# Kernel optimization log

Hardware: AMD Instinct MI355X
Metric: run time of the kernel (lower is better)

The kernel has to match this reference:

```python
import jax, jax.numpy as jnp
import numpy as np

N, D_MODEL, D_FFN, K = 8192, 1024, 4096, 512


def setup_inputs() -> dict:
    key = jax.random.key(0)
    ks = jax.random.split(key, 5)
    x = jax.random.normal(ks[0], (N, D_MODEL), dtype=jnp.float32)
    topk_indices = jax.random.randint(ks[1], (N, K), 0, D_FFN, dtype=jnp.int32)
    scale = 0.02
    w_gate = jax.random.normal(ks[2], (D_MODEL, D_FFN), dtype=jnp.float32) * scale
    w_up = jax.random.normal(ks[3], (D_MODEL, D_FFN), dtype=jnp.float32) * scale
    w_down = jax.random.normal(ks[4], (D_FFN, D_MODEL), dtype=jnp.float32) * scale
    return {"x": x, "topk_indices": topk_indices, "w_gate": w_gate, "w_up": w_up, "w_down": w_down}


def reference(x, topk_indices, w_gate, w_up, w_down):
    # Dense gate/up projections: [N, d_ffn]
    G = x @ w_gate
    U = x @ w_up
    # Gather only the top-k active neurons per token and fuse SwiGLU there.
    G_act = jnp.take_along_axis(G, topk_indices, axis=1)  # [N, k]
    U_act = jnp.take_along_axis(U, topk_indices, axis=1)  # [N, k]
    Z_active = jax.nn.silu(G_act) * U_act                 # [N, k]
    # Sparse-to-dense down projection: scatter active activations back into
    # the d_ffn axis (zeros elsewhere), then dense matmul with w_down.
    n, k = topk_indices.shape
    rows = jnp.arange(n, dtype=topk_indices.dtype)[:, None]
    Z_dense = jnp.zeros((n, w_down.shape[0]), dtype=Z_active.dtype).at[rows, topk_indices].add(Z_active)
    return Z_dense @ w_down  # [N, d_model]
```

## Files before the change

### kernel.cpp

```cpp
#include <hip/hip_runtime.h>
#include <hip/hip_bf16.h>
#include <cstdint>
#include <cstddef>

#define N_TOK   8192
#define D_MODEL 1024
#define D_FFN   4096
#define K_TOP   512
#define NHALF   2048

typedef __bf16 bf16_t;
typedef __bf16 bf16x8 __attribute__((ext_vector_type(8)));
typedef __bf16 bf16x4 __attribute__((ext_vector_type(4)));
typedef float  f32x4  __attribute__((ext_vector_type(4)));


__global__ void cvt_f32_bf16(const float* __restrict__ in, bf16_t* __restrict__ out, int n4) {
  int i = blockIdx.x * blockDim.x + threadIdx.x;
  if (i < n4) {
    const f32x4 v = ((const f32x4*)in)[i];
    bf16x4 o;
    o[0] = (bf16_t)v[0]; o[1] = (bf16_t)v[1]; o[2] = (bf16_t)v[2]; o[3] = (bf16_t)v[3];
    ((bf16x4*)out)[i] = o;
  }
}

__global__ void transpose_cvt(const float* __restrict__ in, bf16_t* __restrict__ out,
                              int rows, int cols) {
  __shared__ float tile[32][33];
  const int tx = threadIdx.x, ty = threadIdx.y;
  const int x = blockIdx.x * 32 + tx;
#pragma unroll
  for (int i = 0; i < 32; i += 8) {
    int y = blockIdx.y * 32 + ty + i;
    tile[ty + i][tx] = in[(size_t)y * cols + x];
  }
  __syncthreads();
  const int xo = blockIdx.y * 32 + tx;
#pragma unroll
  for (int i = 0; i < 32; i += 8) {
    int yo = blockIdx.x * 32 + ty + i;
    out[(size_t)yo * rows + xo] = (bf16_t)tile[tx][ty + i];
  }
}

#define ROWS_PER_BLK 4
__global__ __launch_bounds__(256) void count_scatter_lds(
    const int* __restrict__ idx, unsigned int* __restrict__ M) {
  __shared__ unsigned int loc[ROWS_PER_BLK * (D_FFN / 8)];
  const int t = threadIdx.x;
  const int r0 = blockIdx.x * ROWS_PER_BLK;

#pragma unroll
  for (int i = 0; i < ROWS_PER_BLK * (D_FFN / 8) / 256; ++i)
    loc[t + i * 256] = 0;
  __syncthreads();

  const int* ip = idx + (size_t)r0 * K_TOP;
#pragma unroll
  for (int i = 0; i < ROWS_PER_BLK * K_TOP / 256; ++i) {
    const int e = t + i * 256;
    const int lr = e >> 9;
    const int j = ip[e];
    atomicAdd(&loc[lr * (D_FFN / 8) + (j >> 3)], 1u << ((j & 7) * 4));
  }
  __syncthreads();

  unsigned int* op = M + (size_t)r0 * (D_FFN / 8);
#pragma unroll
  for (int i = 0; i < ROWS_PER_BLK * (D_FFN / 8) / 256; ++i)
    op[t + i * 256] = loc[t + i * 256];
}


__device__ __forceinline__ void gload_lds16(const void* g, void* l) {
#if __has_builtin(__builtin_amdgcn_global_load_lds)
  __builtin_amdgcn_global_load_lds((__attribute__((address_space(1))) void*)(g),
                                   (__attribute__((address_space(3))) void*)(l), 16, 0, 0);
#else
  *(bf16x8*)l = *(const bf16x8*)g;
#endif
}

#define MFMA16(ACC, AF, BF)                                                      \
  _Pragma("unroll")                                                              \
  for (int m = 0; m < 4; ++m)                                                    \
    _Pragma("unroll")                                                            \
    for (int n = 0; n < 4; ++n)                                                  \
      ACC[m][n] = __builtin_amdgcn_mfma_f32_16x16x32_bf16(AF[m], BF[n], ACC[m][n], 0, 0, 0);


#define BM1 256
#define BN1 128
#define BK1 32
#define NT1 (D_MODEL / BK1)
#define GU_BUF 32768

__global__ __launch_bounds__(512, 2) void gemm_gateup_3b(
    const bf16_t* __restrict__ A,
    const bf16_t* __restrict__ Bg,
    const bf16_t* __restrict__ Bu,
    const unsigned int* __restrict__ cnt,
    bf16_t* __restrict__ Z,
    int n_base)
{
  extern __shared__ char smem[];
  const int t = threadIdx.x;
  const int lane = t & 63;
  const int w = t >> 6;
  const int wr = w >> 1;
  const int wc = w & 1;
  const int l15 = lane & 15;
  const int grp = lane >> 4;
  const int m0 = blockIdx.x * BM1;
  const int n0 = blockIdx.y * BN1;

  const int sA0 = t, sA1 = t + 512;
  const int rA0 = sA0 >> 2, uA0 = (sA0 & 3) ^ ((rA0 >> 1) & 3);
  const int rA1 = sA1 >> 2, uA1 = (sA1 & 3) ^ ((rA1 >> 1) & 3);
  const int rB  = t >> 2,   uB  = (t & 3) ^ ((rB >> 1) & 3);
  const int gA0 = (m0 + rA0) * D_MODEL + uA0 * 8;
  const int gA1 = (m0 + rA1) * D_MODEL + uA1 * 8;
  const int gB  = (n_base + n0 + rB) * D_MODEL + uB * 8;
  const int dA0 = sA0 * 16, dA1 = sA1 * 16, dB = t * 16;

#define GU_STAGE(ti) do {                                                        \
    char* _b = smem + ((ti) % 3) * GU_BUF; const int _k = (ti) * BK1;            \
    gload_lds16(A  + gA0 + _k, _b + dA0);                                        \
    gload_lds16(A  + gA1 + _k, _b + dA1);                                        \
    gload_lds16(Bg + gB  + _k, _b + 16384 + dB);                                 \
    gload_lds16(Bu + gB  + _k, _b + 24576 + dB); } while (0)

  int a_off[4], bg_off[4];
#pragma unroll
  for (int m = 0; m < 4; ++m) {
    const int row = wr * 64 + m * 16 + l15;
    a_off[m] = row * 64 + ((grp ^ ((row >> 1) & 3)) * 16);
  }
#pragma unroll
  for (int n = 0; n < 4; ++n) {
    const int row = wc * 64 + n * 16 + l15;
    bg_off[n] = 16384 + row * 64 + ((grp ^ ((row >> 1) & 3)) * 16);
  }

  GU_STAGE(0); GU_STAGE(1);
  asm volatile("s_waitcnt vmcnt(4)" ::: "memory");
  __builtin_amdgcn_s_barrier();

  bf16x8 af[4], bgf[4], buf_[4];
#pragma unroll
  for (int m = 0; m < 4; ++m) af[m] = *(const bf16x8*)(smem + a_off[m]);
#pragma unroll
  for (int n = 0; n < 4; ++n) bgf[n] = *(const bf16x8*)(smem + bg_off[n]);

  f32x4 accg[4][4] = {};
  f32x4 accu[4][4] = {};

  for (int tt = 0; tt < NT1; ++tt) {
    char* rbuf = smem + (tt % 3) * GU_BUF;
    if (tt + 2 < NT1) GU_STAGE(tt + 2);
#pragma unroll
    for (int n = 0; n < 4; ++n) buf_[n] = *(const bf16x8*)(rbuf + bg_off[n] + 8192);
    asm volatile("s_waitcnt lgkmcnt(4)" ::: "memory");
    __builtin_amdgcn_s_setprio(1);
    MFMA16(accg, af, bgf);
    __builtin_amdgcn_s_setprio(0);
    asm volatile("s_waitcnt lgkmcnt(0)" ::: "memory");
    if (tt + 2 < NT1) { asm volatile("s_waitcnt vmcnt(4)" ::: "memory"); }
    else              { asm volatile("s_waitcnt vmcnt(0)" ::: "memory"); }
    __builtin_amdgcn_s_barrier();
    char* nbuf = smem + ((tt + 1) % 3) * GU_BUF;
    if (tt + 1 < NT1) {
#pragma unroll
      for (int n = 0; n < 4; ++n) bgf[n] = *(const bf16x8*)(nbuf + bg_off[n]);
    }
    __builtin_amdgcn_s_setprio(1);
    MFMA16(accu, af, buf_);
    __builtin_amdgcn_s_setprio(0);
    if (tt + 1 < NT1) {
#pragma unroll
      for (int m = 0; m < 4; ++m) af[m] = *(const bf16x8*)(nbuf + a_off[m]);
    }
  }

#pragma unroll
  for (int m = 0; m < 4; ++m) {
#pragma unroll
    for (int n = 0; n < 4; ++n) {
      const int colL = n0 + wc * 64 + n * 16 + l15;
      const int jg = n_base + colL;
#pragma unroll
      for (int j = 0; j < 4; ++j) {
        const int row = m0 + wr * 64 + m * 16 + grp * 4 + j;
        float g = accg[m][n][j];
        float u = accu[m][n][j];
        unsigned int cw = cnt[(size_t)row * (D_FFN / 8) + (jg >> 3)];
        float c = (float)((cw >> ((jg & 7) * 4)) & 15u);
        float z = c * u * (g / (1.0f + __expf(-g)));
        Z[(size_t)row * NHALF + colL] = (bf16_t)z;
      }
    }
  }
#undef GU_STAGE
}

#define BM2 256
#define BN2 128
#define BK2 32
#define NT2 (NHALF / BK2)
#define DN_BUF 24576

__global__ __launch_bounds__(512, 4) void gemm_down_3b(
    const bf16_t* __restrict__ Az,
    const bf16_t* __restrict__ B,
    float* __restrict__ C,
    int k_base, int accum)
{
  extern __shared__ char smem[];
  const int t = threadIdx.x;
  const int lane = t & 63;
  const int w = t >> 6;
  const int wr = w >> 1;
  const int wc = w & 1;
  const int l15 = lane & 15;
  const int grp = lane >> 4;
  const int m0 = blockIdx.x * BM2;
  const int n0 = blockIdx.y * BN2;

  const int sA0 = t, sA1 = t + 512;
  const int rA0 = sA0 >> 2, uA0 = (sA0 & 3) ^ ((rA0 >> 1) & 3);
  const int rA1 = sA1 >> 2, uA1 = (sA1 & 3) ^ ((rA1 >> 1) & 3);
  const int rB  = t >> 2,   uB  = (t & 3) ^ ((rB >> 1) & 3);
  const int gA0 = (m0 + rA0) * NHALF + uA0 * 8;
  const int gA1 = (m0 + rA1) * NHALF + uA1 * 8;
  const int gB  = (n0 + rB) * D_FFN + k_base + uB * 8;
  const int dA0 = sA0 * 16, dA1 = sA1 * 16, dB = t * 16;

#define DN_STAGE(ti) do {                                                        \
    char* _b = smem + ((ti) % 3) * DN_BUF; const int _k = (ti) * BK2;            \
    gload_lds16(Az + gA0 + _k, _b + dA0);                                        \
    gload_lds16(Az + gA1 + _k, _b + dA1);                                        \
    gload_lds16(B  + gB  + _k, _b + 16384 + dB); } while (0)

  int a_off[4], b_off[4];
#pragma unroll
  for (int m = 0; m < 4; ++m) {
    const int row = wr * 64 + m * 16 + l15;
    a_off[m] = row * 64 + ((grp ^ ((row >> 1) & 3)) * 16);
  }
#pragma unroll
  for (int n = 0; n < 4; ++n) {
    const int row = wc * 64 + n * 16 + l15;
    b_off[n] = 16384 + row * 64 + ((grp ^ ((row >> 1) & 3)) * 16);
  }

  DN_STAGE(0); DN_STAGE(1);
  asm volatile("s_waitcnt vmcnt(3)" ::: "memory");
  __builtin_amdgcn_s_barrier();

  bf16x8 af[4], bf[4];
#pragma unroll
  for (int m = 0; m < 4; ++m) af[m] = *(const bf16x8*)(smem + a_off[m]);
#pragma unroll
  for (int n = 0; n < 4; ++n) bf[n] = *(const bf16x8*)(smem + b_off[n]);

  f32x4 acc[4][4] = {};

  for (int tt = 0; tt < NT2; ++tt) {
    if (tt + 2 < NT2) DN_STAGE(tt + 2);
    __builtin_amdgcn_s_setprio(1);
    MFMA16(acc, af, bf);
    __builtin_amdgcn_s_setprio(0);
    asm volatile("s_waitcnt lgkmcnt(0)" ::: "memory");
    if (tt + 2 < NT2) { asm volatile("s_waitcnt vmcnt(3)" ::: "memory"); }
    else              { asm volatile("s_waitcnt vmcnt(0)" ::: "memory"); }
    __builtin_amdgcn_s_barrier();
    if (tt + 1 < NT2) {
      char* nbuf = smem + ((tt + 1) % 3) * DN_BUF;
#pragma unroll
      for (int m = 0; m < 4; ++m) af[m] = *(const bf16x8*)(nbuf + a_off[m]);
#pragma unroll
      for (int n = 0; n < 4; ++n) bf[n] = *(const bf16x8*)(nbuf + b_off[n]);
    }
  }

#pragma unroll
  for (int m = 0; m < 4; ++m) {
#pragma unroll
    for (int n = 0; n < 4; ++n) {
      const int col = n0 + wc * 64 + n * 16 + l15;
#pragma unroll
      for (int j = 0; j < 4; ++j) {
        const int row = m0 + wr * 64 + m * 16 + grp * 4 + j;
        const size_t off = (size_t)row * D_MODEL + col;
        float prev = accum ? C[off] : 0.0f;
        C[off] = prev + acc[m][n][j];
      }
    }
  }
#undef DN_STAGE
}


extern "C" void kernel_launch(void* const* d_in, const int* in_sizes, int n_in,
                              void* d_out, int out_size, void* d_ws, size_t ws_size,
                              hipStream_t stream) {
  const float* x  = (const float*)d_in[0];
  const int*   idx = (const int*)d_in[1];
  const float* wg = (const float*)d_in[2];
  const float* wu = (const float*)d_in[3];
  const float* wd = (const float*)d_in[4];
  float* out = (float*)d_out;

  char* ws = (char*)d_ws;
  const size_t SZ_XB  = (size_t)N_TOK * D_MODEL * 2;
  const size_t SZ_W   = (size_t)D_MODEL * D_FFN * 2;
  const size_t SZ_CNT = (size_t)N_TOK * D_FFN / 2;
  bf16_t* xb  = (bf16_t*)(ws);
  bf16_t* wgT = (bf16_t*)(ws + SZ_XB);
  bf16_t* wuT = (bf16_t*)(ws + SZ_XB + SZ_W);
  bf16_t* wdT = (bf16_t*)(ws + SZ_XB + 2 * SZ_W);
  unsigned int* cnt = (unsigned int*)(ws + SZ_XB + 3 * SZ_W);
  bf16_t* Z   = (bf16_t*)(ws + SZ_XB + 3 * SZ_W + SZ_CNT);

  (void)hipFuncSetAttribute((const void*)gemm_gateup_3b,
                            hipFuncAttributeMaxDynamicSharedMemorySize, 3 * GU_BUF);
  (void)hipFuncSetAttribute((const void*)gemm_down_3b,
                            hipFuncAttributeMaxDynamicSharedMemorySize, 3 * DN_BUF);

  count_scatter_lds<<<N_TOK / ROWS_PER_BLK, 256, 0, stream>>>(idx, cnt);
  cvt_f32_bf16<<<(N_TOK * D_MODEL / 4 + 255) / 256, 256, 0, stream>>>(x, xb, N_TOK * D_MODEL / 4);
  transpose_cvt<<<dim3(D_FFN / 32, D_MODEL / 32), dim3(32, 8), 0, stream>>>(wg, wgT, D_MODEL, D_FFN);
  transpose_cvt<<<dim3(D_FFN / 32, D_MODEL / 32), dim3(32, 8), 0, stream>>>(wu, wuT, D_MODEL, D_FFN);
  transpose_cvt<<<dim3(D_MODEL / 32, D_FFN / 32), dim3(32, 8), 0, stream>>>(wd, wdT, D_FFN, D_MODEL);

  gemm_gateup_3b<<<dim3(N_TOK / BM1, NHALF / BN1), 512, 3 * GU_BUF, stream>>>(xb, wgT, wuT, cnt, Z, 0);
  gemm_down_3b<<<dim3(N_TOK / BM2, D_MODEL / BN2), 512, 3 * DN_BUF, stream>>>(Z, wdT, out, 0, 0);
  gemm_gateup_3b<<<dim3(N_TOK / BM1, NHALF / BN1), 512, 3 * GU_BUF, stream>>>(xb, wgT, wuT, cnt, Z, NHALF);
  gemm_down_3b<<<dim3(N_TOK / BM2, D_MODEL / BN2), 512, 3 * DN_BUF, stream>>>(Z, wdT, out, NHALF, 1);
}
```

Measured before the change: 270.0 us.

## Load A fragments directly from global into registers, stage only B in LDS

Both GEMM kernels stop staging the activation (A) tile through LDS. Each wave now loads its A fragments straight from global memory one iteration ahead, while only the weight tiles go through the triple-buffered LDS ring. The aim is to shrink the LDS footprint and LDS traffic and to move the barrier to the loop head. The cost is that each A element is fetched by both waves sharing a row, and loads are less coalesced with global latency exposed. The down kernel's launch bound is also lowered from 4 to 2 blocks.

```diff
diff --git a/kernel.cpp b/kernel.cpp
--- a/kernel.cpp
+++ b/kernel.cpp
@@ -94,9 +94,9 @@
 #define BN1 128
 #define BK1 32
 #define NT1 (D_MODEL / BK1)
-#define GU_BUF 32768
-
-__global__ __launch_bounds__(512, 2) void gemm_gateup_3b(
+#define GU_BUF 16384
+
+__global__ __launch_bounds__(512, 2) void gemm_gateup_ad(
     const bf16_t* __restrict__ A,
     const bf16_t* __restrict__ Bg,
     const bf16_t* __restrict__ Bu,
@@ -115,41 +115,33 @@
   const int m0 = blockIdx.x * BM1;
   const int n0 = blockIdx.y * BN1;
 
-  const int sA0 = t, sA1 = t + 512;
-  const int rA0 = sA0 >> 2, uA0 = (sA0 & 3) ^ ((rA0 >> 1) & 3);
-  const int rA1 = sA1 >> 2, uA1 = (sA1 & 3) ^ ((rA1 >> 1) & 3);
-  const int rB  = t >> 2,   uB  = (t & 3) ^ ((rB >> 1) & 3);
-  const int gA0 = (m0 + rA0) * D_MODEL + uA0 * 8;
-  const int gA1 = (m0 + rA1) * D_MODEL + uA1 * 8;
-  const int gB  = (n_base + n0 + rB) * D_MODEL + uB * 8;
-  const int dA0 = sA0 * 16, dA1 = sA1 * 16, dB = t * 16;
+  const int rB = t >> 2, uB = (t & 3) ^ ((rB >> 1) & 3);
+  const int gB = (n_base + n0 + rB) * D_MODEL + uB * 8;
+  const int dB = t * 16;
 
 #define GU_STAGE(ti) do {                                                        \
     char* _b = smem + ((ti) % 3) * GU_BUF; const int _k = (ti) * BK1;            \
-    gload_lds16(A  + gA0 + _k, _b + dA0);                                        \
-    gload_lds16(A  + gA1 + _k, _b + dA1);                                        \
-    gload_lds16(Bg + gB  + _k, _b + 16384 + dB);                                 \
-    gload_lds16(Bu + gB  + _k, _b + 24576 + dB); } while (0)
-
-  int a_off[4], bg_off[4];
-#pragma unroll
-  for (int m = 0; m < 4; ++m) {
-    const int row = wr * 64 + m * 16 + l15;
-    a_off[m] = row * 64 + ((grp ^ ((row >> 1) & 3)) * 16);
-  }
+    gload_lds16(Bg + gB + _k, _b + dB);                                          \
+    gload_lds16(Bu + gB + _k, _b + 8192 + dB); } while (0)
+
+  const bf16_t* aP[4];
+#pragma unroll
+  for (int m = 0; m < 4; ++m)
+    aP[m] = A + (size_t)(m0 + wr * 64 + m * 16 + l15) * D_MODEL + grp * 8;
+
+  int bg_off[4];
 #pragma unroll
   for (int n = 0; n < 4; ++n) {
     const int row = wc * 64 + n * 16 + l15;
-    bg_off[n] = 16384 + row * 64 + ((grp ^ ((row >> 1) & 3)) * 16);
+    bg_off[n] = row * 64 + ((grp ^ ((row >> 1) & 3)) * 16);
   }
 
   GU_STAGE(0); GU_STAGE(1);
-  asm volatile("s_waitcnt vmcnt(4)" ::: "memory");
+  bf16x8 af[4], bgf[4];
+#pragma unroll
+  for (int m = 0; m < 4; ++m) af[m] = *(const bf16x8*)(aP[m]);
+  asm volatile("s_waitcnt vmcnt(6)" ::: "memory");
   __builtin_amdgcn_s_barrier();
-
-  bf16x8 af[4], bgf[4], buf_[4];
-#pragma unroll
-  for (int m = 0; m < 4; ++m) af[m] = *(const bf16x8*)(smem + a_off[m]);
 #pragma unroll
   for (int n = 0; n < 4; ++n) bgf[n] = *(const bf16x8*)(smem + bg_off[n]);
 
@@ -158,28 +150,39 @@
 
   for (int tt = 0; tt < NT1; ++tt) {
     char* rbuf = smem + (tt % 3) * GU_BUF;
-    if (tt + 2 < NT1) GU_STAGE(tt + 2);
-#pragma unroll
-    for (int n = 0; n < 4; ++n) buf_[n] = *(const bf16x8*)(rbuf + bg_off[n] + 8192);
+    const bool stg = (tt + 2 < NT1);
+    const bool nxt = (tt + 1 < NT1);
+
+    asm volatile("s_waitcnt vmcnt(4)" ::: "memory");
+    __builtin_amdgcn_s_barrier();
+    if (stg) GU_STAGE(tt + 2);
+    bf16x8 bu_[4];
+#pragma unroll
+    for (int n = 0; n < 4; ++n) bu_[n] = *(const bf16x8*)(rbuf + bg_off[n] + 8192);
     asm volatile("s_waitcnt lgkmcnt(4)" ::: "memory");
     __builtin_amdgcn_s_setprio(1);
     MFMA16(accg, af, bgf);
     __builtin_amdgcn_s_setprio(0);
-    asm volatile("s_waitcnt lgkmcnt(0)" ::: "memory");
-    if (tt + 2 < NT1) { asm volatile("s_waitcnt vmcnt(4)" ::: "memory"); }
-    else              { asm volatile("s_waitcnt vmcnt(0)" ::: "memory"); }
-    __builtin_amdgcn_s_barrier();
-    char* nbuf = smem + ((tt + 1) % 3) * GU_BUF;
-    if (tt + 1 < NT1) {
-#pragma unroll
-      for (int n = 0; n < 4; ++n) bgf[n] = *(const bf16x8*)(nbuf + bg_off[n]);
+
+    bf16x8 afN[4], bgfN[4];
+    if (nxt) {
+      char* nbuf = smem + ((tt + 1) % 3) * GU_BUF;
+#pragma unroll
+      for (int n = 0; n < 4; ++n) bgfN[n] = *(const bf16x8*)(nbuf + bg_off[n]);
+#pragma unroll
+      for (int m = 0; m < 4; ++m) afN[m] = *(const bf16x8*)(aP[m] + (tt + 1) * BK1);
+      asm volatile("s_waitcnt lgkmcnt(4)" ::: "memory");
+    } else {
+      asm volatile("s_waitcnt lgkmcnt(0)" ::: "memory");
     }
     __builtin_amdgcn_s_setprio(1);
-    MFMA16(accu, af, buf_);
+    MFMA16(accu, af, bu_);
     __builtin_amdgcn_s_setprio(0);
-    if (tt + 1 < NT1) {
-#pragma unroll
-      for (int m = 0; m < 4; ++m) af[m] = *(const bf16x8*)(nbuf + a_off[m]);
+    if (nxt) {
+#pragma unroll
+      for (int m = 0; m < 4; ++m) af[m] = afN[m];
+#pragma unroll
+      for (int n = 0; n < 4; ++n) bgf[n] = bgfN[n];
     }
   }
 
@@ -208,9 +211,9 @@
 #define BN2 128
 #define BK2 32
 #define NT2 (NHALF / BK2)
-#define DN_BUF 24576
-
-__global__ __launch_bounds__(512, 4) void gemm_down_3b(
+#define DN_BUF 8192
+
+__global__ __launch_bounds__(512, 2) void gemm_down_ad(
     const bf16_t* __restrict__ Az,
     const bf16_t* __restrict__ B,
     float* __restrict__ C,
@@ -227,60 +230,61 @@
   const int m0 = blockIdx.x * BM2;
   const int n0 = blockIdx.y * BN2;
 
-  const int sA0 = t, sA1 = t + 512;
-  const int rA0 = sA0 >> 2, uA0 = (sA0 & 3) ^ ((rA0 >> 1) & 3);
-  const int rA1 = sA1 >> 2, uA1 = (sA1 & 3) ^ ((rA1 >> 1) & 3);
-  const int rB  = t >> 2,   uB  = (t & 3) ^ ((rB >> 1) & 3);
-  const int gA0 = (m0 + rA0) * NHALF + uA0 * 8;
-  const int gA1 = (m0 + rA1) * NHALF + uA1 * 8;
-  const int gB  = (n0 + rB) * D_FFN + k_base + uB * 8;
-  const int dA0 = sA0 * 16, dA1 = sA1 * 16, dB = t * 16;
+  const int rB = t >> 2, uB = (t & 3) ^ ((rB >> 1) & 3);
+  const int gB = (n0 + rB) * D_FFN + k_base + uB * 8;
+  const int dB = t * 16;
 
 #define DN_STAGE(ti) do {                                                        \
-    char* _b = smem + ((ti) % 3) * DN_BUF; const int _k = (ti) * BK2;            \
-    gload_lds16(Az + gA0 + _k, _b + dA0);                                        \
-    gload_lds16(Az + gA1 + _k, _b + dA1);                                        \
-    gload_lds16(B  + gB  + _k, _b + 16384 + dB); } while (0)
-
-  int a_off[4], b_off[4];
-#pragma unroll
-  for (int m = 0; m < 4; ++m) {
-    const int row = wr * 64 + m * 16 + l15;
-    a_off[m] = row * 64 + ((grp ^ ((row >> 1) & 3)) * 16);
-  }
+    gload_lds16(B + gB + (ti) * BK2, smem + ((ti) % 3) * DN_BUF + dB); } while (0)
+
+  const bf16_t* aP[4];
+#pragma unroll
+  for (int m = 0; m < 4; ++m)
+    aP[m] = Az + (size_t)(m0 + wr * 64 + m * 16 + l15) * NHALF + grp * 8;
+
+  int b_off[4];
 #pragma unroll
   for (int n = 0; n < 4; ++n) {
     const int row = wc * 64 + n * 16 + l15;
-    b_off[n] = 16384 + row * 64 + ((grp ^ ((row >> 1) & 3)) * 16);
+    b_off[n] = row * 64 + ((grp ^ ((row >> 1) & 3)) * 16);
   }
 
   DN_STAGE(0); DN_STAGE(1);
-  asm volatile("s_waitcnt vmcnt(3)" ::: "memory");
+  bf16x8 af[4], bf[4];
+#pragma unroll
+  for (int m = 0; m < 4; ++m) af[m] = *(const bf16x8*)(aP[m]);
+  asm volatile("s_waitcnt vmcnt(5)" ::: "memory");
   __builtin_amdgcn_s_barrier();
-
-  bf16x8 af[4], bf[4];
-#pragma unroll
-  for (int m = 0; m < 4; ++m) af[m] = *(const bf16x8*)(smem + a_off[m]);
 #pragma unroll
   for (int n = 0; n < 4; ++n) bf[n] = *(const bf16x8*)(smem + b_off[n]);
 
   f32x4 acc[4][4] = {};
 
   for (int tt = 0; tt < NT2; ++tt) {
-    if (tt + 2 < NT2) DN_STAGE(tt + 2);
+    const bool stg = (tt + 2 < NT2);
+    const bool nxt = (tt + 1 < NT2);
+
+    asm volatile("s_waitcnt vmcnt(4)" ::: "memory");
+    __builtin_amdgcn_s_barrier();
+    if (stg) DN_STAGE(tt + 2);
+    asm volatile("s_waitcnt lgkmcnt(0)" ::: "memory");
+
+    bf16x8 afN[4], bfN[4];
+    if (nxt) {
+      char* nbuf = smem + ((tt + 1) % 3) * DN_BUF;
+#pragma unroll
+      for (int n = 0; n < 4; ++n) bfN[n] = *(const bf16x8*)(nbuf + b_off[n]);
+#pragma unroll
+      for (int m = 0; m < 4; ++m) afN[m] = *(const bf16x8*)(aP[m] + (tt + 1) * BK2);
+    }
     __builtin_amdgcn_s_setprio(1);
     MFMA16(acc, af, bf);
     __builtin_amdgcn_s_setprio(0);
-    asm volatile("s_waitcnt lgkmcnt(0)" ::: "memory");
-    if (tt + 2 < NT2) { asm volatile("s_waitcnt vmcnt(3)" ::: "memory"); }
-    else              { asm volatile("s_waitcnt vmcnt(0)" ::: "memory"); }
-    __builtin_amdgcn_s_barrier();
-    if (tt + 1 < NT2) {
-      char* nbuf = smem + ((tt + 1) % 3) * DN_BUF;
-#pragma unroll
-      for (int m = 0; m < 4; ++m) af[m] = *(const bf16x8*)(nbuf + a_off[m]);
-#pragma unroll
-      for (int n = 0; n < 4; ++n) bf[n] = *(const bf16x8*)(nbuf + b_off[n]);
+    if (nxt) {
+#pragma unroll
+      for (int m = 0; m < 4; ++m) af[m] = afN[m];
+#pragma unroll
+      for (int n = 0; n < 4; ++n) bf[n] = bfN[n];
     }
   }
 
@@ -323,9 +327,9 @@
   unsigned int* cnt = (unsigned int*)(ws + SZ_XB + 3 * SZ_W);
   bf16_t* Z   = (bf16_t*)(ws + SZ_XB + 3 * SZ_W + SZ_CNT);
 
-  (void)hipFuncSetAttribute((const void*)gemm_gateup_3b,
+  (void)hipFuncSetAttribute((const void*)gemm_gateup_ad,
                             hipFuncAttributeMaxDynamicSharedMemorySize, 3 * GU_BUF);
-  (void)hipFuncSetAttribute((const void*)gemm_down_3b,
+  (void)hipFuncSetAttribute((const void*)gemm_down_ad,
                             hipFuncAttributeMaxDynamicSharedMemorySize, 3 * DN_BUF);
 
   count_scatter_lds<<<N_TOK / ROWS_PER_BLK, 256, 0, stream>>>(idx, cnt);
@@ -334,8 +338,8 @@
   transpose_cvt<<<dim3(D_FFN / 32, D_MODEL / 32), dim3(32, 8), 0, stream>>>(wu, wuT, D_MODEL, D_FFN);
   transpose_cvt<<<dim3(D_MODEL / 32, D_FFN / 32), dim3(32, 8), 0, stream>>>(wd, wdT, D_FFN, D_MODEL);
 
-  gemm_gateup_3b<<<dim3(N_TOK / BM1, NHALF / BN1), 512, 3 * GU_BUF, stream>>>(xb, wgT, wuT, cnt, Z, 0);
-  gemm_down_3b<<<dim3(N_TOK / BM2, D_MODEL / BN2), 512, 3 * DN_BUF, stream>>>(Z, wdT, out, 0, 0);
-  gemm_gateup_3b<<<dim3(N_TOK / BM1, NHALF / BN1), 512, 3 * GU_BUF, stream>>>(xb, wgT, wuT, cnt, Z, NHALF);
-  gemm_down_3b<<<dim3(N_TOK / BM2, D_MODEL / BN2), 512, 3 * DN_BUF, stream>>>(Z, wdT, out, NHALF, 1);
-}
+  gemm_gateup_ad<<<dim3(N_TOK / BM1, NHALF / BN1), 512, 3 * GU_BUF, stream>>>(xb, wgT, wuT, cnt, Z, 0);
+  gemm_down_ad<<<dim3(N_TOK / BM2, D_MODEL / BN2), 512, 3 * DN_BUF, stream>>>(Z, wdT, out, 0, 0);
+  gemm_gateup_ad<<<dim3(N_TOK / BM1, NHALF / BN1), 512, 3 * GU_BUF, stream>>>(xb, wgT, wuT, cnt, Z, NHALF);
+  gemm_down_ad<<<dim3(N_TOK / BM2, D_MODEL / BN2), 512, 3 * DN_BUF, stream>>>(Z, wdT, out, NHALF, 1);
+}
```

Result: slower. 447.8 us (+65.9%).

## Restructure down-projection GEMM to double-buffered BK=64 pipeline with split-K sub-steps

Applied to the files above, without the earlier changes.

Replaces the triple-buffered BK=32 down-projection kernel with a double-buffered BK=64 variant. Each iteration prefetches the next tile and runs two MFMA sub-steps from the current LDS buffer, with barriers and sched_barrier fences controlling interleaving. It uses an 8-way XOR swizzle for the wider rows. The goal is fewer loop iterations and barrier/wait overheads per unit of MFMA work, at the cost of more LDS per block (96KB) and lower occupancy (launch bounds 2 instead of 4). It also adds extra barriers that could serialize waves.

```diff
diff --git a/kernel.cpp b/kernel.cpp
--- a/kernel.cpp
+++ b/kernel.cpp
@@ -206,12 +206,12 @@
 
 #define BM2 256
 #define BN2 128
-#define BK2 32
+#define BK2 64
 #define NT2 (NHALF / BK2)
-#define DN_BUF 24576
-
-__global__ __launch_bounds__(512, 4) void gemm_down_3b(
-    const bf16_t* __restrict__ Az,
+#define LDSBUF2 49152
+
+__global__ __launch_bounds__(512, 2) void gemm_down_8p(
+    const bf16_t* __restrict__ A,
     const bf16_t* __restrict__ B,
     float* __restrict__ C,
     int k_base, int accum)
@@ -227,61 +227,75 @@
   const int m0 = blockIdx.x * BM2;
   const int n0 = blockIdx.y * BN2;
 
-  const int sA0 = t, sA1 = t + 512;
-  const int rA0 = sA0 >> 2, uA0 = (sA0 & 3) ^ ((rA0 >> 1) & 3);
-  const int rA1 = sA1 >> 2, uA1 = (sA1 & 3) ^ ((rA1 >> 1) & 3);
-  const int rB  = t >> 2,   uB  = (t & 3) ^ ((rB >> 1) & 3);
-  const int gA0 = (m0 + rA0) * NHALF + uA0 * 8;
-  const int gA1 = (m0 + rA1) * NHALF + uA1 * 8;
-  const int gB  = (n0 + rB) * D_FFN + k_base + uB * 8;
-  const int dA0 = sA0 * 16, dA1 = sA1 * 16, dB = t * 16;
-
-#define DN_STAGE(ti) do {                                                        \
-    char* _b = smem + ((ti) % 3) * DN_BUF; const int _k = (ti) * BK2;            \
-    gload_lds16(Az + gA0 + _k, _b + dA0);                                        \
-    gload_lds16(Az + gA1 + _k, _b + dA1);                                        \
-    gload_lds16(B  + gB  + _k, _b + 16384 + dB); } while (0)
-
-  int a_off[4], b_off[4];
-#pragma unroll
-  for (int m = 0; m < 4; ++m) {
-    const int row = wr * 64 + m * 16 + l15;
-    a_off[m] = row * 64 + ((grp ^ ((row >> 1) & 3)) * 16);
-  }
-#pragma unroll
-  for (int n = 0; n < 4; ++n) {
-    const int row = wc * 64 + n * 16 + l15;
-    b_off[n] = 16384 + row * 64 + ((grp ^ ((row >> 1) & 3)) * 16);
-  }
-
-  DN_STAGE(0); DN_STAGE(1);
-  asm volatile("s_waitcnt vmcnt(3)" ::: "memory");
-  __builtin_amdgcn_s_barrier();
-
-  bf16x8 af[4], bf[4];
-#pragma unroll
-  for (int m = 0; m < 4; ++m) af[m] = *(const bf16x8*)(smem + a_off[m]);
-#pragma unroll
-  for (int n = 0; n < 4; ++n) bf[n] = *(const bf16x8*)(smem + b_off[n]);
+  int offA[4], offB[2];
+#pragma unroll
+  for (int c = 0; c < 4; ++c) {
+    const int s = c * 512 + w * 64 + lane;
+    const int r = s >> 3, cb = (s & 7) ^ (r & 7);
+    offA[c] = (m0 + r) * NHALF + cb * 8;
+  }
+#pragma unroll
+  for (int c = 0; c < 2; ++c) {
+    const int s = c * 512 + w * 64 + lane;
+    const int r = s >> 3, cb = (s & 7) ^ (r & 7);
+    offB[c] = (n0 + r) * D_FFN + k_base + cb * 8;
+  }
+  const int dst0 = (w * 64 + lane) * 16;
+
+  const int swz = l15 & 7;
+  const int a_k0 = wr * 8192 + l15 * 128 + ((0 + grp) ^ swz) * 16;
+  const int a_k1 = wr * 8192 + l15 * 128 + ((4 + grp) ^ swz) * 16;
+  const int b_k0 = 32768 + wc * 8192 + l15 * 128 + ((0 + grp) ^ swz) * 16;
+  const int b_k1 = 32768 + wc * 8192 + l15 * 128 + ((4 + grp) ^ swz) * 16;
+
+#pragma unroll
+  for (int c = 0; c < 4; ++c) gload_lds16(A + offA[c], smem + dst0 + c * 8192);
+#pragma unroll
+  for (int c = 0; c < 2; ++c) gload_lds16(B + offB[c], smem + 32768 + dst0 + c * 8192);
 
   f32x4 acc[4][4] = {};
 
   for (int tt = 0; tt < NT2; ++tt) {
-    if (tt + 2 < NT2) DN_STAGE(tt + 2);
+    char* rb = smem + (tt & 1) * LDSBUF2;
+    char* wb = smem + ((tt & 1) ^ 1) * LDSBUF2;
+    const int kg = (tt + 1) * BK2;
+    const bool st = (tt + 1 < NT2);
+    bf16x8 af[4], bf[4];
+
+    if (st) {
+#pragma unroll
+      for (int c = 0; c < 4; ++c) gload_lds16(A + offA[c] + kg, wb + dst0 + c * 8192);
+#pragma unroll
+      for (int c = 0; c < 2; ++c) gload_lds16(B + offB[c] + kg, wb + 32768 + dst0 + c * 8192);
+      asm volatile("s_waitcnt vmcnt(6)" ::: "memory");
+    } else {
+      asm volatile("s_waitcnt vmcnt(0)" ::: "memory");
+    }
+    __builtin_amdgcn_s_barrier();
+
+#pragma unroll
+    for (int m = 0; m < 4; ++m) af[m] = *(const bf16x8*)(rb + a_k0 + m * 2048);
+#pragma unroll
+    for (int n = 0; n < 4; ++n) bf[n] = *(const bf16x8*)(rb + b_k0 + n * 2048);
+    __builtin_amdgcn_s_barrier();
+    asm volatile("s_waitcnt lgkmcnt(0)" ::: "memory");
+    __builtin_amdgcn_sched_barrier(0);
     __builtin_amdgcn_s_setprio(1);
     MFMA16(acc, af, bf);
     __builtin_amdgcn_s_setprio(0);
+    __builtin_amdgcn_s_barrier();
+
+#pragma unroll
+    for (int m = 0; m < 4; ++m) af[m] = *(const bf16x8*)(rb + a_k1 + m * 2048);
+#pragma unroll
+    for (int n = 0; n < 4; ++n) bf[n] = *(const bf16x8*)(rb + b_k1 + n * 2048);
+    __builtin_amdgcn_s_barrier();
     asm volatile("s_waitcnt lgkmcnt(0)" ::: "memory");
-    if (tt + 2 < NT2) { asm volatile("s_waitcnt vmcnt(3)" ::: "memory"); }
-    else              { asm volatile("s_waitcnt vmcnt(0)" ::: "memory"); }
-    __builtin_amdgcn_s_barrier();
-    if (tt + 1 < NT2) {
-      char* nbuf = smem + ((tt + 1) % 3) * DN_BUF;
-#pragma unroll
-      for (int m = 0; m < 4; ++m) af[m] = *(const bf16x8*)(nbuf + a_off[m]);
-#pragma unroll
-      for (int n = 0; n < 4; ++n) bf[n] = *(const bf16x8*)(nbuf + b_off[n]);
-    }
+    __builtin_amdgcn_sched_barrier(0);
+    __builtin_amdgcn_s_setprio(1);
+    MFMA16(acc, af, bf);
+    __builtin_amdgcn_s_setprio(0);
+    __builtin_amdgcn_s_barrier();
   }
 
 #pragma unroll
@@ -298,7 +312,6 @@
       }
     }
   }
-#undef DN_STAGE
 }
 
 
@@ -325,8 +338,8 @@
 
   (void)hipFuncSetAttribute((const void*)gemm_gateup_3b,
                             hipFuncAttributeMaxDynamicSharedMemorySize, 3 * GU_BUF);
-  (void)hipFuncSetAttribute((const void*)gemm_down_3b,
-                            hipFuncAttributeMaxDynamicSharedMemorySize, 3 * DN_BUF);
+  (void)hipFuncSetAttribute((const void*)gemm_down_8p,
+                            hipFuncAttributeMaxDynamicSharedMemorySize, 2 * LDSBUF2);
 
   count_scatter_lds<<<N_TOK / ROWS_PER_BLK, 256, 0, stream>>>(idx, cnt);
   cvt_f32_bf16<<<(N_TOK * D_MODEL / 4 + 255) / 256, 256, 0, stream>>>(x, xb, N_TOK * D_MODEL / 4);
@@ -335,7 +348,7 @@
   transpose_cvt<<<dim3(D_MODEL / 32, D_FFN / 32), dim3(32, 8), 0, stream>>>(wd, wdT, D_FFN, D_MODEL);
 
   gemm_gateup_3b<<<dim3(N_TOK / BM1, NHALF / BN1), 512, 3 * GU_BUF, stream>>>(xb, wgT, wuT, cnt, Z, 0);
-  gemm_down_3b<<<dim3(N_TOK / BM2, D_MODEL / BN2), 512, 3 * DN_BUF, stream>>>(Z, wdT, out, 0, 0);
+  gemm_down_8p<<<dim3(N_TOK / BM2, D_MODEL / BN2), 512, 2 * LDSBUF2, stream>>>(Z, wdT, out, 0, 0);
   gemm_gateup_3b<<<dim3(N_TOK / BM1, NHALF / BN1), 512, 3 * GU_BUF, stream>>>(xb, wgT, wuT, cnt, Z, NHALF);
-  gemm_down_3b<<<dim3(N_TOK / BM2, D_MODEL / BN2), 512, 3 * DN_BUF, stream>>>(Z, wdT, out, NHALF, 1);
-}
+  gemm_down_8p<<<dim3(N_TOK / BM2, D_MODEL / BN2), 512, 2 * LDSBUF2, stream>>>(Z, wdT, out, NHALF, 1);
+}
```

Measured after the change: 279.3 us. +3.4%, slower.

## Use full-width Z when workspace allows and shrink down-proj tile to 128 rows

Applied to the files above, without the earlier changes.

When the workspace is large enough, the gate/up GEMM writes the full 4096-wide Z in one launch and the down projection runs one pass over K=4096. This removes the second pair of launches and the read-modify-write accumulation into the fp32 output. The down GEMM tile shrinks from 256 to 128 rows, which gives more blocks and fewer registers per wave. Its loop is reordered so the next LDS fragments load before the MFMAs. The cost is a Z buffer twice as large and lower reuse of the B tile per block.

```diff
diff --git a/kernel.cpp b/kernel.cpp
--- a/kernel.cpp
+++ b/kernel.cpp
@@ -89,7 +89,6 @@
     for (int n = 0; n < 4; ++n)                                                  \
       ACC[m][n] = __builtin_amdgcn_mfma_f32_16x16x32_bf16(AF[m], BF[n], ACC[m][n], 0, 0, 0);
 
-
 #define BM1 256
 #define BN1 128
 #define BK1 32
@@ -102,7 +101,7 @@
     const bf16_t* __restrict__ Bu,
     const unsigned int* __restrict__ cnt,
     bf16_t* __restrict__ Z,
-    int n_base)
+    int n_base, int zstride)
 {
   extern __shared__ char smem[];
   const int t = threadIdx.x;
@@ -197,24 +196,23 @@
         unsigned int cw = cnt[(size_t)row * (D_FFN / 8) + (jg >> 3)];
         float c = (float)((cw >> ((jg & 7) * 4)) & 15u);
         float z = c * u * (g / (1.0f + __expf(-g)));
-        Z[(size_t)row * NHALF + colL] = (bf16_t)z;
+        Z[(size_t)row * zstride + colL] = (bf16_t)z;
       }
     }
   }
 #undef GU_STAGE
 }
 
-#define BM2 256
+#define BM2 128
 #define BN2 128
 #define BK2 32
-#define NT2 (NHALF / BK2)
-#define DN_BUF 24576
+#define DN_BUF 16384
 
 __global__ __launch_bounds__(512, 4) void gemm_down_3b(
-    const bf16_t* __restrict__ Az,
+    const bf16_t* __restrict__ A,
     const bf16_t* __restrict__ B,
     float* __restrict__ C,
-    int k_base, int accum)
+    int k_base, int accum, int zstride, int ntk)
 {
   extern __shared__ char smem[];
   const int t = threadIdx.x;
@@ -227,71 +225,80 @@
   const int m0 = blockIdx.x * BM2;
   const int n0 = blockIdx.y * BN2;
 
-  const int sA0 = t, sA1 = t + 512;
-  const int rA0 = sA0 >> 2, uA0 = (sA0 & 3) ^ ((rA0 >> 1) & 3);
-  const int rA1 = sA1 >> 2, uA1 = (sA1 & 3) ^ ((rA1 >> 1) & 3);
-  const int rB  = t >> 2,   uB  = (t & 3) ^ ((rB >> 1) & 3);
-  const int gA0 = (m0 + rA0) * NHALF + uA0 * 8;
-  const int gA1 = (m0 + rA1) * NHALF + uA1 * 8;
-  const int gB  = (n0 + rB) * D_FFN + k_base + uB * 8;
-  const int dA0 = sA0 * 16, dA1 = sA1 * 16, dB = t * 16;
+  const int rS = t >> 2, uS = (t & 3) ^ ((rS >> 1) & 3);
+  const int gA = (m0 + rS) * zstride + uS * 8;
+  const int gB = (n0 + rS) * D_FFN + k_base + uS * 8;
+  const int dS = t * 16;
 
 #define DN_STAGE(ti) do {                                                        \
     char* _b = smem + ((ti) % 3) * DN_BUF; const int _k = (ti) * BK2;            \
-    gload_lds16(Az + gA0 + _k, _b + dA0);                                        \
-    gload_lds16(Az + gA1 + _k, _b + dA1);                                        \
-    gload_lds16(B  + gB  + _k, _b + 16384 + dB); } while (0)
-
-  int a_off[4], b_off[4];
-#pragma unroll
-  for (int m = 0; m < 4; ++m) {
-    const int row = wr * 64 + m * 16 + l15;
+    gload_lds16(A + gA + _k, _b + dS);                                           \
+    gload_lds16(B + gB + _k, _b + 8192 + dS); } while (0)
+
+  int a_off[2], b_off[4];
+#pragma unroll
+  for (int m = 0; m < 2; ++m) {
+    const int row = wr * 32 + m * 16 + l15;
     a_off[m] = row * 64 + ((grp ^ ((row >> 1) & 3)) * 16);
   }
 #pragma unroll
   for (int n = 0; n < 4; ++n) {
     const int row = wc * 64 + n * 16 + l15;
-    b_off[n] = 16384 + row * 64 + ((grp ^ ((row >> 1) & 3)) * 16);
+    b_off[n] = 8192 + row * 64 + ((grp ^ ((row >> 1) & 3)) * 16);
   }
 
   DN_STAGE(0); DN_STAGE(1);
-  asm volatile("s_waitcnt vmcnt(3)" ::: "memory");
+  asm volatile("s_waitcnt vmcnt(2)" ::: "memory");
   __builtin_amdgcn_s_barrier();
 
-  bf16x8 af[4], bf[4];
-#pragma unroll
-  for (int m = 0; m < 4; ++m) af[m] = *(const bf16x8*)(smem + a_off[m]);
+  bf16x8 af[2], bf[4];
+#pragma unroll
+  for (int m = 0; m < 2; ++m) af[m] = *(const bf16x8*)(smem + a_off[m]);
 #pragma unroll
   for (int n = 0; n < 4; ++n) bf[n] = *(const bf16x8*)(smem + b_off[n]);
 
-  f32x4 acc[4][4] = {};
-
-  for (int tt = 0; tt < NT2; ++tt) {
-    if (tt + 2 < NT2) DN_STAGE(tt + 2);
+  f32x4 acc[2][4] = {};
+
+  for (int tt = 0; tt < ntk; ++tt) {
+    const bool st2 = (tt + 2 < ntk);
+    const bool nxt = (tt + 1 < ntk);
+    if (st2) DN_STAGE(tt + 2);
+    if (st2) { asm volatile("s_waitcnt vmcnt(2)" ::: "memory"); }
+    else     { asm volatile("s_waitcnt vmcnt(0)" ::: "memory"); }
+    __builtin_amdgcn_s_barrier();
+
+    bf16x8 afN[2], bfN[4];
+    if (nxt) {
+      char* nbuf = smem + ((tt + 1) % 3) * DN_BUF;
+#pragma unroll
+      for (int m = 0; m < 2; ++m) afN[m] = *(const bf16x8*)(nbuf + a_off[m]);
+#pragma unroll
+      for (int n = 0; n < 4; ++n) bfN[n] = *(const bf16x8*)(nbuf + b_off[n]);
+    }
     __builtin_amdgcn_s_setprio(1);
-    MFMA16(acc, af, bf);
+#pragma unroll
+    for (int m = 0; m < 2; ++m)
+#pragma unroll
+      for (int n = 0; n < 4; ++n)
+        acc[m][n] = __builtin_amdgcn_mfma_f32_16x16x32_bf16(af[m], bf[n], acc[m][n], 0, 0, 0);
     __builtin_amdgcn_s_setprio(0);
     asm volatile("s_waitcnt lgkmcnt(0)" ::: "memory");
-    if (tt + 2 < NT2) { asm volatile("s_waitcnt vmcnt(3)" ::: "memory"); }
-    else              { asm volatile("s_waitcnt vmcnt(0)" ::: "memory"); }
-    __builtin_amdgcn_s_barrier();
-    if (tt + 1 < NT2) {
-      char* nbuf = smem + ((tt + 1) % 3) * DN_BUF;
-#pragma unroll
-      for (int m = 0; m < 4; ++m) af[m] = *(const bf16x8*)(nbuf + a_off[m]);
-#pragma unroll
-      for (int n = 0; n < 4; ++n) bf[n] = *(const bf16x8*)(nbuf + b_off[n]);
-    }
-  }
-
-#pragma unroll
-  for (int m = 0; m < 4; ++m) {
+    if (nxt) {
+#pragma unroll
+      for (int m = 0; m < 2; ++m) af[m] = afN[m];
+#pragma unroll
+      for (int n = 0; n < 4; ++n) bf[n] = bfN[n];
+    }
+  }
+
+#pragma unroll
+  for (int m = 0; m < 2; ++m) {
 #pragma unroll
     for (int n = 0; n < 4; ++n) {
       const int col = n0 + wc * 64 + n * 16 + l15;
 #pragma unroll
       for (int j = 0; j < 4; ++j) {
-        const int row = m0 + wr * 64 + m * 16 + grp * 4 + j;
+        const int row = m0 + wr * 32 + m * 16 + grp * 4 + j;
         const size_t off = (size_t)row * D_MODEL + col;
         float prev = accum ? C[off] : 0.0f;
         C[off] = prev + acc[m][n][j];
@@ -316,12 +323,17 @@
   const size_t SZ_XB  = (size_t)N_TOK * D_MODEL * 2;
   const size_t SZ_W   = (size_t)D_MODEL * D_FFN * 2;
   const size_t SZ_CNT = (size_t)N_TOK * D_FFN / 2;
+  const size_t SZ_ZF  = (size_t)N_TOK * D_FFN * 2;
+  const size_t SZ_ZH  = (size_t)N_TOK * NHALF * 2;
   bf16_t* xb  = (bf16_t*)(ws);
   bf16_t* wgT = (bf16_t*)(ws + SZ_XB);
   bf16_t* wuT = (bf16_t*)(ws + SZ_XB + SZ_W);
   bf16_t* wdT = (bf16_t*)(ws + SZ_XB + 2 * SZ_W);
   unsigned int* cnt = (unsigned int*)(ws + SZ_XB + 3 * SZ_W);
   bf16_t* Z   = (bf16_t*)(ws + SZ_XB + 3 * SZ_W + SZ_CNT);
+  const size_t WS_FULL = SZ_XB + 3 * SZ_W + SZ_CNT + SZ_ZF;
+  const bool full = (ws_size >= WS_FULL);
+  (void)SZ_ZH;
 
   (void)hipFuncSetAttribute((const void*)gemm_gateup_3b,
                             hipFuncAttributeMaxDynamicSharedMemorySize, 3 * GU_BUF);
@@ -334,8 +346,19 @@
   transpose_cvt<<<dim3(D_FFN / 32, D_MODEL / 32), dim3(32, 8), 0, stream>>>(wu, wuT, D_MODEL, D_FFN);
   transpose_cvt<<<dim3(D_MODEL / 32, D_FFN / 32), dim3(32, 8), 0, stream>>>(wd, wdT, D_FFN, D_MODEL);
 
-  gemm_gateup_3b<<<dim3(N_TOK / BM1, NHALF / BN1), 512, 3 * GU_BUF, stream>>>(xb, wgT, wuT, cnt, Z, 0);
-  gemm_down_3b<<<dim3(N_TOK / BM2, D_MODEL / BN2), 512, 3 * DN_BUF, stream>>>(Z, wdT, out, 0, 0);
-  gemm_gateup_3b<<<dim3(N_TOK / BM1, NHALF / BN1), 512, 3 * GU_BUF, stream>>>(xb, wgT, wuT, cnt, Z, NHALF);
-  gemm_down_3b<<<dim3(N_TOK / BM2, D_MODEL / BN2), 512, 3 * DN_BUF, stream>>>(Z, wdT, out, NHALF, 1);
-}
+  if (full) {
+    gemm_gateup_3b<<<dim3(N_TOK / BM1, D_FFN / BN1), 512, 3 * GU_BUF, stream>>>(
+        xb, wgT, wuT, cnt, Z, 0, D_FFN);
+    gemm_down_3b<<<dim3(N_TOK / BM2, D_MODEL / BN2), 512, 3 * DN_BUF, stream>>>(
+        Z, wdT, out, 0, 0, D_FFN, D_FFN / BK2);
+  } else {
+    gemm_gateup_3b<<<dim3(N_TOK / BM1, NHALF / BN1), 512, 3 * GU_BUF, stream>>>(
+        xb, wgT, wuT, cnt, Z, 0, NHALF);
+    gemm_down_3b<<<dim3(N_TOK / BM2, D_MODEL / BN2), 512, 3 * DN_BUF, stream>>>(
+        Z, wdT, out, 0, 0, NHALF, NHALF / BK2);
+    gemm_gateup_3b<<<dim3(N_TOK / BM1, NHALF / BN1), 512, 3 * GU_BUF, stream>>>(
+        xb, wgT, wuT, cnt, Z, NHALF, NHALF);
+    gemm_down_3b<<<dim3(N_TOK / BM2, D_MODEL / BN2), 512, 3 * DN_BUF, stream>>>(
+        Z, wdT, out, NHALF, 1, NHALF, NHALF / BK2);
+  }
+}
```

After: 269.3 us. Within noise of the previous version (-0.3%).
